# Kernel optimization log

Hardware: AMD Instinct MI355X
Metric: run time of the kernel (lower is better)

The kernel has to match this reference:

```python
import jax, jax.numpy as jnp
import numpy as np

T, B, I, H = 512, 64, 1024, 1024


def setup_inputs() -> dict:
    key = jax.random.key(0)
    ks = jax.random.split(key, 9)
    u = lambda k, shape: jax.random.uniform(k, shape, jnp.float32, -0.05, 0.05)
    return {
        "x": jax.random.normal(ks[0], (T, B, I), jnp.float32),
        "h0": jnp.zeros((B, H), jnp.float32),
        "c0": jnp.zeros((B, H), jnp.float32),
        "W_f": u(ks[1], (I + H, H)), "b_f": u(ks[2], (H,)),
        "W_i": u(ks[3], (I + H, H)), "b_i": u(ks[4], (H,)),
        "W_C": u(ks[5], (I + H, H)), "b_C": u(ks[6], (H,)),
        "W_o": u(ks[7], (I + H, H)), "b_o": u(ks[8], (H,)),
    }


def reference(x, h0, c0, W_f, b_f, W_i, b_i, W_C, b_C, W_o, b_o):
    # Fuse the 4 gate projections into one GEMM: W is [(H_prev + I), 4H]
    W = jnp.concatenate([W_f, W_i, W_C, W_o], axis=1)  # [I+H, 4H]
    b = jnp.concatenate([b_f, b_i, b_C, b_o], axis=0)  # [4H]
    Hn = h0.shape[1]

    def step(carry, x_t):
        h_t1, c_t1 = carry
        xh = jnp.concatenate([h_t1, x_t], axis=1)  # [B, H+I]
        gates = xh @ W + b                          # [B, 4H]
        f_t = jax.nn.sigmoid(gates[:, 0 * Hn:1 * Hn])
        i_t = jax.nn.sigmoid(gates[:, 1 * Hn:2 * Hn])
        g_t = jnp.tanh(gates[:, 2 * Hn:3 * Hn])
        o_t = jax.nn.sigmoid(gates[:, 3 * Hn:4 * Hn])
        c_t = f_t * c_t1 + i_t * g_t
        h_t = o_t * jnp.tanh(c_t)
        return (h_t, c_t), h_t

    (h_last, c_last), h_seq = jax.lax.scan(step, (h0, c0), x)
    return h_seq, h_last, c_last
```

## Files before the change

kernel.cpp:

```cpp
#include <hip/hip_runtime.h>

typedef unsigned short u16;
typedef unsigned int   u32;
typedef unsigned long long u64;
typedef __attribute__((ext_vector_type(8))) __bf16 bf16x8;
typedef __attribute__((ext_vector_type(4))) float  f32x4;

#define NWG    128
#define TSTEPS 512

__device__ __forceinline__ u16 f2bf(float f) {
  union { float f; u32 u; } v; v.f = f;
  return (u16)((v.u + 0x7FFFu + ((v.u >> 16) & 1u)) >> 16);
}
__device__ __forceinline__ float sigf(float x)     { return 1.f / (1.f + __expf(-x)); }
__device__ __forceinline__ float tanhfast(float x) { return 2.f / (1.f + __expf(-2.f * x)) - 1.f; }

__global__ void convert_x_kernel(const float* __restrict__ x, u16* __restrict__ xb, long n) {
  long i = (long)(blockIdx.x * blockDim.x + threadIdx.x) * 4;
  long stride = (long)gridDim.x * blockDim.x * 4;
  for (; i < n; i += stride) {
    float4 v = *reinterpret_cast<const float4*>(x + i);
    ushort4 o; o.x = f2bf(v.x); o.y = f2bf(v.y); o.z = f2bf(v.z); o.w = f2bf(v.w);
    *reinterpret_cast<ushort4*>(xb + i) = o;
  }
}

__global__ void convert_h0_tiled(const float* __restrict__ h0, u16* __restrict__ hb) {
  int gid = blockIdx.x * blockDim.x + threadIdx.x;
  int row = gid >> 9;
  int k0  = (gid & 511) << 1;
  float a = h0[row * 1024 + k0];
  float b = h0[row * 1024 + k0 + 1];
  int off = ((row >> 4) * 32 + (k0 >> 5)) * 512 + (row & 15) * 32 + ((k0 >> 3) & 3) * 8 + (k0 & 7);
  u32 hv = (u32)f2bf(a) | ((u32)f2bf(b) << 16);
  *((u32*)hb + (off >> 1)) = hv;
}

__global__ void arrange_w_kernel(const float* __restrict__ Wf, const float* __restrict__ Wi,
                                 const float* __restrict__ Wc, const float* __restrict__ Wo,
                                 u16* __restrict__ wfrag) {
  __shared__ float lds[4][512][8];
  const int n = blockIdx.x >> 2;
  const int w = blockIdx.x & 3;
  const int tid = threadIdx.x;
  #pragma unroll
  for (int g = 0; g < 4; ++g) {
    const float* W = (g == 0) ? Wf : (g == 1) ? Wi : (g == 2) ? Wc : Wo;
    for (int it = 0; it < 16; ++it) {
      int e = it * 256 + tid;
      int kk = e >> 3, jj = e & 7;
      lds[g][kk][jj] = W[(size_t)(w * 512 + kk) * 1024 + n * 8 + jj];
    }
  }
  __syncthreads();
  u16* outp = wfrag + ((size_t)blockIdx.x << 14);
  for (int it = 0; it < 64; ++it) {
    int e = it * 256 + tid;
    int b = e & 7, lane = (e >> 3) & 63, tile = (e >> 9) & 1, ks = e >> 10;
    int kk = ks * 32 + ((lane >> 4) << 3) + b;
    int c  = tile * 16 + (lane & 15);
    int g  = c >> 3, jj = c & 7;
    outp[e] = f2bf(lds[g][kk][jj]);
  }
}

__launch_bounds__(256, 1)
__global__ void lstm_main_kernel(
    const u16* __restrict__ xbf, const u16* __restrict__ wfrag,
    const float* __restrict__ c0,
    const float* __restrict__ bF, const float* __restrict__ bI,
    const float* __restrict__ bC, const float* __restrict__ bO,
    u16* __restrict__ hb, float* __restrict__ out, u32* flags)
{
  const int n    = blockIdx.x;
  const int tid  = threadIdx.x;
  const int w    = tid >> 6;
  const int lane = tid & 63;
  const int lr   = lane & 15;
  const int hi   = lane >> 4;
  const int lk   = hi << 3;

  __shared__ float part[4][64][36];

  bf16x8 bq[16][2];
  {
    const u16* wp = wfrag + ((size_t)(n * 4 + w) << 14) + lane * 8;
    #pragma unroll
    for (int ks = 0; ks < 16; ++ks) {
      bq[ks][0] = *reinterpret_cast<const bf16x8*>(wp + ks * 1024);
      bq[ks][1] = *reinterpret_cast<const bf16x8*>(wp + ks * 1024 + 512);
    }
  }

  const int erow = tid >> 2;
  const int ejj  = (tid & 3) << 1;
  const int j0   = n * 8 + ejj;
  float cR0 = c0[erow * 1024 + j0];
  float cR1 = c0[erow * 1024 + j0 + 1];
  const float bf0 = bF[j0], bf1 = bF[j0 + 1];
  const float bi0 = bI[j0], bi1 = bI[j0 + 1];
  const float bc0 = bC[j0], bc1 = bC[j0 + 1];
  const float bo0 = bO[j0], bo1 = bO[j0 + 1];
  const int hoff_u32 = (((erow >> 4) * 32 + (j0 >> 5)) * 512
                        + (erow & 15) * 32 + ((j0 >> 3) & 3) * 8 + (j0 & 7)) >> 1;

  #pragma unroll 1
  for (int t = 0; t < TSTEPS; ++t) {
    f32x4 acc[4][2];
    #pragma unroll
    for (int m = 0; m < 4; ++m) {
      acc[m][0] = (f32x4){0.f, 0.f, 0.f, 0.f};
      acc[m][1] = (f32x4){0.f, 0.f, 0.f, 0.f};
    }

    if (w < 2) {
      if (t > 0) {
        const u32 tv = (u32)t;
        while (true) {
          u32 f0 = __hip_atomic_load(flags + lane,      __ATOMIC_RELAXED, __HIP_MEMORY_SCOPE_AGENT);
          u32 f1 = __hip_atomic_load(flags + 64 + lane, __ATOMIC_RELAXED, __HIP_MEMORY_SCOPE_AGENT);
          if (__all((f0 >= tv) && (f1 >= tv))) break;
          __builtin_amdgcn_s_sleep(1);
        }
      }
      const u64* hq = (const u64*)(hb + (t & 1) * 65536);
      #pragma unroll
      for (int m = 0; m < 4; ++m) {
        union { u64 q[2]; bf16x8 v; } av[16];
        #pragma unroll
        for (int ks = 0; ks < 16; ++ks) {
          int idx = (m * 32 + w * 16 + ks) * 128 + lr * 8 + hi * 2;
          av[ks].q[0] = __hip_atomic_load(hq + idx,     __ATOMIC_RELAXED, __HIP_MEMORY_SCOPE_AGENT);
          av[ks].q[1] = __hip_atomic_load(hq + idx + 1, __ATOMIC_RELAXED, __HIP_MEMORY_SCOPE_AGENT);
        }
        #pragma unroll
        for (int ks = 0; ks < 16; ++ks) {
          acc[m][0] = __builtin_amdgcn_mfma_f32_16x16x32_bf16(av[ks].v, bq[ks][0], acc[m][0], 0, 0, 0);
          acc[m][1] = __builtin_amdgcn_mfma_f32_16x16x32_bf16(av[ks].v, bq[ks][1], acc[m][1], 0, 0, 0);
        }
      }
    } else {
      const u16* asrc = xbf + (size_t)t * 65536 + (w - 2) * 512;
      #pragma unroll
      for (int ks = 0; ks < 16; ++ks) {
        #pragma unroll
        for (int m = 0; m < 4; ++m) {
          bf16x8 av = *reinterpret_cast<const bf16x8*>(asrc + (m * 16 + lr) * 1024 + ks * 32 + lk);
          acc[m][0] = __builtin_amdgcn_mfma_f32_16x16x32_bf16(av, bq[ks][0], acc[m][0], 0, 0, 0);
          acc[m][1] = __builtin_amdgcn_mfma_f32_16x16x32_bf16(av, bq[ks][1], acc[m][1], 0, 0, 0);
        }
      }
    }

    #pragma unroll
    for (int m = 0; m < 4; ++m)
      #pragma unroll
      for (int nt = 0; nt < 2; ++nt)
        #pragma unroll
        for (int r = 0; r < 4; ++r)
          part[w][m * 16 + (hi << 2) + r][nt * 16 + lr] = acc[m][nt][r];

    __syncthreads();

    float a8[8];
    #pragma unroll
    for (int q = 0; q < 2; ++q) {
      int jj = ejj + q;
      #pragma unroll
      for (int g = 0; g < 4; ++g)
        a8[q * 4 + g] = part[0][erow][g * 8 + jj] + part[1][erow][g * 8 + jj]
                      + part[2][erow][g * 8 + jj] + part[3][erow][g * 8 + jj];
    }
    float fA = sigf(a8[0] + bf0), iA = sigf(a8[1] + bi0);
    float gA = tanhfast(a8[2] + bc0), oA = sigf(a8[3] + bo0);
    float cn0 = fA * cR0 + iA * gA;
    float hn0 = oA * tanhfast(cn0);
    cR0 = cn0;
    float fB = sigf(a8[4] + bf1), iB = sigf(a8[5] + bi1);
    float gB = tanhfast(a8[6] + bc1), oB = sigf(a8[7] + bo1);
    float cn1 = fB * cR1 + iB * gB;
    float hn1 = oB * tanhfast(cn1);
    cR1 = cn1;

    {
      u32 hv = (u32)f2bf(hn0) | ((u32)f2bf(hn1) << 16);
      u32* hdst32 = (u32*)(hb + ((t + 1) & 1) * 65536) + hoff_u32;
      __hip_atomic_store(hdst32, hv, __ATOMIC_RELAXED, __HIP_MEMORY_SCOPE_AGENT);
    }
    size_t ob = (size_t)t * 65536 + erow * 1024 + j0;
    out[ob]     = hn0;
    out[ob + 1] = hn1;
    if (t == TSTEPS - 1) {
      out[33554432 + erow * 1024 + j0]     = hn0;
      out[33554432 + erow * 1024 + j0 + 1] = hn1;
      out[33619968 + erow * 1024 + j0]     = cn0;
      out[33619968 + erow * 1024 + j0 + 1] = cn1;
    }

    __syncthreads();
    if (t < TSTEPS - 1 && tid == 0)
      __hip_atomic_store(flags + n, (u32)(t + 1), __ATOMIC_RELAXED, __HIP_MEMORY_SCOPE_AGENT);
  }
}

extern "C" void kernel_launch(void* const* d_in, const int* in_sizes, int n_in,
                              void* d_out, int out_size, void* d_ws, size_t ws_size,
                              hipStream_t stream) {
  const float* x  = (const float*)d_in[0];
  const float* h0 = (const float*)d_in[1];
  const float* c0 = (const float*)d_in[2];
  const float* Wf = (const float*)d_in[3];
  const float* bf = (const float*)d_in[4];
  const float* Wi = (const float*)d_in[5];
  const float* bi = (const float*)d_in[6];
  const float* Wc = (const float*)d_in[7];
  const float* bc = (const float*)d_in[8];
  const float* Wo = (const float*)d_in[9];
  const float* bo = (const float*)d_in[10];

  if (ws_size < ((80u << 20) + (1u << 18) + 1024)) return;
  char* ws   = (char*)d_ws;
  u16* wfrag = (u16*)ws;
  u16* xbf   = (u16*)(ws + (16u << 20));
  u16* hb    = (u16*)(ws + (80u << 20));
  u32* flags = (u32*)(ws + (80u << 20) + (1u << 18));
  float* outp = (float*)d_out;

  hipMemsetAsync(flags, 0, 512, stream);
  convert_x_kernel<<<2048, 256, 0, stream>>>(x, xbf, (long)512 * 64 * 1024);
  convert_h0_tiled<<<128, 256, 0, stream>>>(h0, hb);
  arrange_w_kernel<<<512, 256, 0, stream>>>(Wf, Wi, Wc, Wo, wfrag);

  void* args[] = {(void*)&xbf, (void*)&wfrag, (void*)&c0, (void*)&bf, (void*)&bi,
                  (void*)&bc, (void*)&bo, (void*)&hb, (void*)&outp, (void*)&flags};
  hipError_t e = hipLaunchCooperativeKernel((const void*)lstm_main_kernel, dim3(NWG),
                                            dim3(256), args, 0, stream);
  if (e != hipSuccess) {
    lstm_main_kernel<<<dim3(NWG), dim3(256), 0, stream>>>(xbf, wfrag, c0, bf, bi,
                                                          bc, bo, hb, outp, flags);
  }
}
```

Before: 5.838 ms.

## Add dedicated aggregator workgroup to publish per-step epoch for grid barrier

Adds an extra workgroup whose first wavefront polls all 128 per-workgroup flags and publishes a single epoch counter each timestep. Compute workgroups now have one wave spin on that single epoch word and relay readiness to the second wave through an LDS variable, instead of two waves each scanning 128 flags. This is meant to cut global-memory polling traffic and contention on the flag array. The cost is an extra hop of latency through the aggregator on every step and one more workgroup in the cooperative launch.

```diff
diff --git a/kernel.cpp b/kernel.cpp
--- a/kernel.cpp
+++ b/kernel.cpp
@@ -75,6 +75,24 @@
 {
   const int n    = blockIdx.x;
   const int tid  = threadIdx.x;
+  u32* const epoch = flags + 192;
+
+  if (n == NWG) {
+    if (tid < 64) {
+      for (u32 tv = 1; tv < TSTEPS; ++tv) {
+        while (true) {
+          u32 f0 = __hip_atomic_load(flags + tid,      __ATOMIC_RELAXED, __HIP_MEMORY_SCOPE_AGENT);
+          u32 f1 = __hip_atomic_load(flags + 64 + tid, __ATOMIC_RELAXED, __HIP_MEMORY_SCOPE_AGENT);
+          if (__all((f0 >= tv) && (f1 >= tv))) break;
+          __builtin_amdgcn_s_sleep(1);
+        }
+        if (tid == 0)
+          __hip_atomic_store(epoch, tv, __ATOMIC_RELAXED, __HIP_MEMORY_SCOPE_AGENT);
+      }
+    }
+    return;
+  }
+
   const int w    = tid >> 6;
   const int lane = tid & 63;
   const int lr   = lane & 15;
@@ -82,6 +100,7 @@
   const int lk   = hi << 3;
 
   __shared__ float part[4][64][36];
+  __shared__ u32 go;
 
   bf16x8 bq[16][2];
   {
@@ -92,6 +111,8 @@
       bq[ks][1] = *reinterpret_cast<const bf16x8*>(wp + ks * 1024 + 512);
     }
   }
+  if (tid == 0) go = 0;
+  __syncthreads();
 
   const int erow = tid >> 2;
   const int ejj  = (tid & 3) << 1;
@@ -117,11 +138,14 @@
     if (w < 2) {
       if (t > 0) {
         const u32 tv = (u32)t;
-        while (true) {
-          u32 f0 = __hip_atomic_load(flags + lane,      __ATOMIC_RELAXED, __HIP_MEMORY_SCOPE_AGENT);
-          u32 f1 = __hip_atomic_load(flags + 64 + lane, __ATOMIC_RELAXED, __HIP_MEMORY_SCOPE_AGENT);
-          if (__all((f0 >= tv) && (f1 >= tv))) break;
-          __builtin_amdgcn_s_sleep(1);
+        if (w == 0) {
+          while (__hip_atomic_load(epoch, __ATOMIC_RELAXED, __HIP_MEMORY_SCOPE_AGENT) < tv)
+            __builtin_amdgcn_s_sleep(4);
+          if (lane == 0)
+            __hip_atomic_store(&go, tv, __ATOMIC_RELAXED, __HIP_MEMORY_SCOPE_WORKGROUP);
+        } else {
+          while (__hip_atomic_load(&go, __ATOMIC_RELAXED, __HIP_MEMORY_SCOPE_WORKGROUP) < tv)
+            __builtin_amdgcn_s_sleep(1);
         }
       }
       const u64* hq = (const u64*)(hb + (t & 1) * 65536);
@@ -227,17 +251,17 @@
   u32* flags = (u32*)(ws + (80u << 20) + (1u << 18));
   float* outp = (float*)d_out;
 
-  hipMemsetAsync(flags, 0, 512, stream);
+  hipMemsetAsync(flags, 0, 1024, stream);
   convert_x_kernel<<<2048, 256, 0, stream>>>(x, xbf, (long)512 * 64 * 1024);
   convert_h0_tiled<<<128, 256, 0, stream>>>(h0, hb);
   arrange_w_kernel<<<512, 256, 0, stream>>>(Wf, Wi, Wc, Wo, wfrag);
 
   void* args[] = {(void*)&xbf, (void*)&wfrag, (void*)&c0, (void*)&bf, (void*)&bi,
                   (void*)&bc, (void*)&bo, (void*)&hb, (void*)&outp, (void*)&flags};
-  hipError_t e = hipLaunchCooperativeKernel((const void*)lstm_main_kernel, dim3(NWG),
+  hipError_t e = hipLaunchCooperativeKernel((const void*)lstm_main_kernel, dim3(NWG + 1),
                                             dim3(256), args, 0, stream);
   if (e != hipSuccess) {
-    lstm_main_kernel<<<dim3(NWG), dim3(256), 0, stream>>>(xbf, wfrag, c0, bf, bi,
-                                                          bc, bo, hb, outp, flags);
-  }
-}
+    lstm_main_kernel<<<dim3(NWG + 1), dim3(256), 0, stream>>>(xbf, wfrag, c0, bf, bi,
+                                                              bc, bo, hb, outp, flags);
+  }
+}
```

Result: faster. 5.316 ms (-8.9%).

## Replace per-block flag array with global arrival counter and intra-block done flags

Applied to the files above, without the earlier changes.

Replaces the per-workgroup flag array, which every waiter polled across 128 entries, with a single global counter that each workgroup atomically increments once its four waves have stored h. One wave polls the counter and signals the others through an LDS variable. The end-of-step __syncthreads is removed by double-buffering the LDS partial-sum array and using per-wave done flags. The aim is lower grid-barrier latency per timestep. The trade-off is contention on one atomic and relaxed-ordering memory visibility that is easy to get subtly wrong.

```diff
diff --git a/kernel.cpp b/kernel.cpp
--- a/kernel.cpp
+++ b/kernel.cpp
@@ -80,8 +80,11 @@
   const int lr   = lane & 15;
   const int hi   = lane >> 4;
   const int lk   = hi << 3;
-
-  __shared__ float part[4][64][36];
+  u32* const cnt = flags;
+
+  __shared__ float part[2][4][64][36];
+  __shared__ u32 done[4];
+  __shared__ u32 go;
 
   bf16x8 bq[16][2];
   {
@@ -92,6 +95,8 @@
       bq[ks][1] = *reinterpret_cast<const bf16x8*>(wp + ks * 1024 + 512);
     }
   }
+  if (tid < 4) done[tid] = 0;
+  if (tid == 0) go = 0;
 
   const int erow = tid >> 2;
   const int ejj  = (tid & 3) << 1;
@@ -104,9 +109,11 @@
   const float bo0 = bO[j0], bo1 = bO[j0 + 1];
   const int hoff_u32 = (((erow >> 4) * 32 + (j0 >> 5)) * 512
                         + (erow & 15) * 32 + ((j0 >> 3) & 3) * 8 + (j0 & 7)) >> 1;
+  __syncthreads();
 
   #pragma unroll 1
   for (int t = 0; t < TSTEPS; ++t) {
+    const int par = t & 1;
     f32x4 acc[4][2];
     #pragma unroll
     for (int m = 0; m < 4; ++m) {
@@ -116,15 +123,18 @@
 
     if (w < 2) {
       if (t > 0) {
-        const u32 tv = (u32)t;
-        while (true) {
-          u32 f0 = __hip_atomic_load(flags + lane,      __ATOMIC_RELAXED, __HIP_MEMORY_SCOPE_AGENT);
-          u32 f1 = __hip_atomic_load(flags + 64 + lane, __ATOMIC_RELAXED, __HIP_MEMORY_SCOPE_AGENT);
-          if (__all((f0 >= tv) && (f1 >= tv))) break;
-          __builtin_amdgcn_s_sleep(1);
-        }
-      }
-      const u64* hq = (const u64*)(hb + (t & 1) * 65536);
+        const u32 need = (u32)t * (u32)NWG;
+        if (w == 0) {
+          while (__hip_atomic_load(cnt, __ATOMIC_RELAXED, __HIP_MEMORY_SCOPE_AGENT) < need)
+            __builtin_amdgcn_s_sleep(2);
+          if (lane == 0)
+            __hip_atomic_store(&go, (u32)t, __ATOMIC_RELAXED, __HIP_MEMORY_SCOPE_WORKGROUP);
+        } else {
+          while (__hip_atomic_load(&go, __ATOMIC_RELAXED, __HIP_MEMORY_SCOPE_WORKGROUP) < (u32)t)
+            __builtin_amdgcn_s_sleep(1);
+        }
+      }
+      const u64* hq = (const u64*)(hb + par * 65536);
       #pragma unroll
       for (int m = 0; m < 4; ++m) {
         union { u64 q[2]; bf16x8 v; } av[16];
@@ -159,7 +169,7 @@
       for (int nt = 0; nt < 2; ++nt)
         #pragma unroll
         for (int r = 0; r < 4; ++r)
-          part[w][m * 16 + (hi << 2) + r][nt * 16 + lr] = acc[m][nt][r];
+          part[par][w][m * 16 + (hi << 2) + r][nt * 16 + lr] = acc[m][nt][r];
 
     __syncthreads();
 
@@ -169,8 +179,8 @@
       int jj = ejj + q;
       #pragma unroll
       for (int g = 0; g < 4; ++g)
-        a8[q * 4 + g] = part[0][erow][g * 8 + jj] + part[1][erow][g * 8 + jj]
-                      + part[2][erow][g * 8 + jj] + part[3][erow][g * 8 + jj];
+        a8[q * 4 + g] = part[par][0][erow][g * 8 + jj] + part[par][1][erow][g * 8 + jj]
+                      + part[par][2][erow][g * 8 + jj] + part[par][3][erow][g * 8 + jj];
     }
     float fA = sigf(a8[0] + bf0), iA = sigf(a8[1] + bi0);
     float gA = tanhfast(a8[2] + bc0), oA = sigf(a8[3] + bo0);
@@ -185,9 +195,25 @@
 
     {
       u32 hv = (u32)f2bf(hn0) | ((u32)f2bf(hn1) << 16);
-      u32* hdst32 = (u32*)(hb + ((t + 1) & 1) * 65536) + hoff_u32;
+      u32* hdst32 = (u32*)(hb + (par ^ 1) * 65536) + hoff_u32;
       __hip_atomic_store(hdst32, hv, __ATOMIC_RELAXED, __HIP_MEMORY_SCOPE_AGENT);
     }
+
+    if (t < TSTEPS - 1) {
+      asm volatile("s_waitcnt vmcnt(0)" ::: "memory");
+      __builtin_amdgcn_sched_barrier(0);
+      if (lane == 0)
+        __hip_atomic_store(&done[w], (u32)(t + 1), __ATOMIC_RELAXED, __HIP_MEMORY_SCOPE_WORKGROUP);
+      if (w == 3 && lane == 0) {
+        const u32 tv = (u32)(t + 1);
+        while (__hip_atomic_load(&done[0], __ATOMIC_RELAXED, __HIP_MEMORY_SCOPE_WORKGROUP) < tv ||
+               __hip_atomic_load(&done[1], __ATOMIC_RELAXED, __HIP_MEMORY_SCOPE_WORKGROUP) < tv ||
+               __hip_atomic_load(&done[2], __ATOMIC_RELAXED, __HIP_MEMORY_SCOPE_WORKGROUP) < tv)
+          ;
+        __hip_atomic_fetch_add(cnt, 1u, __ATOMIC_RELAXED, __HIP_MEMORY_SCOPE_AGENT);
+      }
+    }
+
     size_t ob = (size_t)t * 65536 + erow * 1024 + j0;
     out[ob]     = hn0;
     out[ob + 1] = hn1;
@@ -197,10 +223,6 @@
       out[33619968 + erow * 1024 + j0]     = cn0;
       out[33619968 + erow * 1024 + j0 + 1] = cn1;
     }
-
-    __syncthreads();
-    if (t < TSTEPS - 1 && tid == 0)
-      __hip_atomic_store(flags + n, (u32)(t + 1), __ATOMIC_RELAXED, __HIP_MEMORY_SCOPE_AGENT);
   }
 }
 
@@ -227,7 +249,7 @@
   u32* flags = (u32*)(ws + (80u << 20) + (1u << 18));
   float* outp = (float*)d_out;
 
-  hipMemsetAsync(flags, 0, 512, stream);
+  hipMemsetAsync(flags, 0, 1024, stream);
   convert_x_kernel<<<2048, 256, 0, stream>>>(x, xbf, (long)512 * 64 * 1024);
   convert_h0_tiled<<<128, 256, 0, stream>>>(h0, hb);
   arrange_w_kernel<<<512, 256, 0, stream>>>(Wf, Wi, Wc, Wo, wfrag);
```

Result: slower. 7.827 ms (+34.1%).

## Add per-XCD relay blocks that copy the hidden state into an XCD-local buffer

Applied to the files above, without the earlier changes.

Launches 64 extra relay workgroups. Up to 8 per XCD wait for all compute blocks to finish a step, copy the bf16 hidden state into a per-XCD buffer, and publish a tag. Compute blocks poll their XCD's tags and, if ready, read h from the copy through sc0 loads. This is meant to cut cross-XCD coherence traffic on the recurrent read, and they fall back to the global flag barrier after a bounded wait. The flag store is also moved ahead of the output writes, adding a relay hop of latency per step and relying on non-atomic copies being visible.

```diff
diff --git a/kernel.cpp b/kernel.cpp
--- a/kernel.cpp
+++ b/kernel.cpp
@@ -7,6 +7,7 @@
 typedef __attribute__((ext_vector_type(4))) float  f32x4;
 
 #define NWG    128
+#define NRELAY 64
 #define TSTEPS 512
 
 __device__ __forceinline__ u16 f2bf(float f) {
@@ -71,10 +72,49 @@
     const float* __restrict__ c0,
     const float* __restrict__ bF, const float* __restrict__ bI,
     const float* __restrict__ bC, const float* __restrict__ bO,
-    u16* __restrict__ hb, float* __restrict__ out, u32* flags)
+    u16* __restrict__ hb, float* __restrict__ out, u32* flags, u16* xcdbuf)
 {
   const int n    = blockIdx.x;
   const int tid  = threadIdx.x;
+  u32* const rcount = flags + 128;
+  u32* const tags   = flags + 256;
+
+  u32 xcd;
+  asm volatile("s_getreg_b32 %0, hwreg(HW_REG_XCC_ID)" : "=s"(xcd));
+  xcd &= 7;
+
+  if (n >= NWG) {
+    __shared__ u32 rr;
+    if (tid == 0)
+      rr = __hip_atomic_fetch_add(rcount + xcd, 1u, __ATOMIC_RELAXED, __HIP_MEMORY_SCOPE_AGENT);
+    __syncthreads();
+    const u32 rank = rr;
+    if (tid >= 64 || rank >= 8) return;
+    const int r = (int)rank;
+    for (int s = 1; s < TSTEPS; ++s) {
+      const u32 sv = (u32)s;
+      while (true) {
+        u32 f0 = __hip_atomic_load(flags + tid,      __ATOMIC_RELAXED, __HIP_MEMORY_SCOPE_AGENT);
+        u32 f1 = __hip_atomic_load(flags + 64 + tid, __ATOMIC_RELAXED, __HIP_MEMORY_SCOPE_AGENT);
+        if (__all((f0 >= sv) && (f1 >= sv))) break;
+        __builtin_amdgcn_s_sleep(2);
+      }
+      const u64* src = (const u64*)(hb + (s & 1) * 65536) + r * 2048;
+      u64* dst = (u64*)(xcdbuf + ((size_t)xcd * 2 + (s & 1)) * 65536) + r * 2048;
+      #pragma unroll
+      for (int i = 0; i < 16; ++i) {
+        int e = (i * 64 + tid) * 2;
+        u64 a = __hip_atomic_load(src + e,     __ATOMIC_RELAXED, __HIP_MEMORY_SCOPE_AGENT);
+        u64 b = __hip_atomic_load(src + e + 1, __ATOMIC_RELAXED, __HIP_MEMORY_SCOPE_AGENT);
+        dst[e] = a; dst[e + 1] = b;
+      }
+      asm volatile("s_waitcnt vmcnt(0)" ::: "memory");
+      if (tid == 0)
+        *(volatile u32*)(tags + xcd * 16 + r) = sv + 1;
+    }
+    return;
+  }
+
   const int w    = tid >> 6;
   const int lane = tid & 63;
   const int lr   = lane & 15;
@@ -82,7 +122,6 @@
   const int lk   = hi << 3;
 
   __shared__ float part[4][64][36];
-
   bf16x8 bq[16][2];
   {
     const u16* wp = wfrag + ((size_t)(n * 4 + w) << 14) + lane * 8;
@@ -115,29 +154,61 @@
     }
 
     if (w < 2) {
+      bool use_local = false;
       if (t > 0) {
-        const u32 tv = (u32)t;
-        while (true) {
-          u32 f0 = __hip_atomic_load(flags + lane,      __ATOMIC_RELAXED, __HIP_MEMORY_SCOPE_AGENT);
-          u32 f1 = __hip_atomic_load(flags + 64 + lane, __ATOMIC_RELAXED, __HIP_MEMORY_SCOPE_AGENT);
-          if (__all((f0 >= tv) && (f1 >= tv))) break;
+        const u32 tv1 = (u32)t + 1;
+        const u32* tagp = tags + xcd * 16 + (lane & 7);
+        for (int tries = 0; tries < 64; ++tries) {
+          u32 tg;
+          asm volatile("global_load_dword %0, %1, off sc0" : "=v"(tg) : "v"(tagp));
+          asm volatile("s_waitcnt vmcnt(0)" ::: "memory");
+          if (__all(tg >= tv1)) { use_local = true; break; }
           __builtin_amdgcn_s_sleep(1);
         }
-      }
-      const u64* hq = (const u64*)(hb + (t & 1) * 65536);
-      #pragma unroll
-      for (int m = 0; m < 4; ++m) {
-        union { u64 q[2]; bf16x8 v; } av[16];
+        if (!use_local) {
+          const u32 tv = (u32)t;
+          while (true) {
+            u32 f0 = __hip_atomic_load(flags + lane,      __ATOMIC_RELAXED, __HIP_MEMORY_SCOPE_AGENT);
+            u32 f1 = __hip_atomic_load(flags + 64 + lane, __ATOMIC_RELAXED, __HIP_MEMORY_SCOPE_AGENT);
+            if (__all((f0 >= tv) && (f1 >= tv))) break;
+            __builtin_amdgcn_s_sleep(2);
+          }
+        }
+      }
+      if (use_local) {
+        const u16* xb = xcdbuf + ((size_t)xcd * 2 + (t & 1)) * 65536;
         #pragma unroll
-        for (int ks = 0; ks < 16; ++ks) {
-          int idx = (m * 32 + w * 16 + ks) * 128 + lr * 8 + hi * 2;
-          av[ks].q[0] = __hip_atomic_load(hq + idx,     __ATOMIC_RELAXED, __HIP_MEMORY_SCOPE_AGENT);
-          av[ks].q[1] = __hip_atomic_load(hq + idx + 1, __ATOMIC_RELAXED, __HIP_MEMORY_SCOPE_AGENT);
-        }
+        for (int m = 0; m < 4; ++m) {
+          bf16x8 av[16];
+          #pragma unroll
+          for (int ks = 0; ks < 16; ++ks)
+            asm volatile("global_load_dwordx4 %0, %1, off sc0"
+                         : "=v"(av[ks])
+                         : "v"(xb + (m * 32 + w * 16 + ks) * 512 + lr * 32 + hi * 8));
+          asm volatile("s_waitcnt vmcnt(0)" ::: "memory");
+          __builtin_amdgcn_sched_barrier(0);
+          #pragma unroll
+          for (int ks = 0; ks < 16; ++ks) {
+            acc[m][0] = __builtin_amdgcn_mfma_f32_16x16x32_bf16(av[ks], bq[ks][0], acc[m][0], 0, 0, 0);
+            acc[m][1] = __builtin_amdgcn_mfma_f32_16x16x32_bf16(av[ks], bq[ks][1], acc[m][1], 0, 0, 0);
+          }
+        }
+      } else {
+        const u64* hq = (const u64*)(hb + (t & 1) * 65536);
         #pragma unroll
-        for (int ks = 0; ks < 16; ++ks) {
-          acc[m][0] = __builtin_amdgcn_mfma_f32_16x16x32_bf16(av[ks].v, bq[ks][0], acc[m][0], 0, 0, 0);
-          acc[m][1] = __builtin_amdgcn_mfma_f32_16x16x32_bf16(av[ks].v, bq[ks][1], acc[m][1], 0, 0, 0);
+        for (int m = 0; m < 4; ++m) {
+          union { u64 q[2]; bf16x8 v; } av[16];
+          #pragma unroll
+          for (int ks = 0; ks < 16; ++ks) {
+            int idx = (m * 32 + w * 16 + ks) * 128 + lr * 8 + hi * 2;
+            av[ks].q[0] = __hip_atomic_load(hq + idx,     __ATOMIC_RELAXED, __HIP_MEMORY_SCOPE_AGENT);
+            av[ks].q[1] = __hip_atomic_load(hq + idx + 1, __ATOMIC_RELAXED, __HIP_MEMORY_SCOPE_AGENT);
+          }
+          #pragma unroll
+          for (int ks = 0; ks < 16; ++ks) {
+            acc[m][0] = __builtin_amdgcn_mfma_f32_16x16x32_bf16(av[ks].v, bq[ks][0], acc[m][0], 0, 0, 0);
+            acc[m][1] = __builtin_amdgcn_mfma_f32_16x16x32_bf16(av[ks].v, bq[ks][1], acc[m][1], 0, 0, 0);
+          }
         }
       }
     } else {
@@ -188,6 +259,11 @@
       u32* hdst32 = (u32*)(hb + ((t + 1) & 1) * 65536) + hoff_u32;
       __hip_atomic_store(hdst32, hv, __ATOMIC_RELAXED, __HIP_MEMORY_SCOPE_AGENT);
     }
+
+    __syncthreads();
+    if (t < TSTEPS - 1 && tid == 0)
+      __hip_atomic_store(flags + n, (u32)(t + 1), __ATOMIC_RELAXED, __HIP_MEMORY_SCOPE_AGENT);
+
     size_t ob = (size_t)t * 65536 + erow * 1024 + j0;
     out[ob]     = hn0;
     out[ob + 1] = hn1;
@@ -197,10 +273,6 @@
       out[33619968 + erow * 1024 + j0]     = cn0;
       out[33619968 + erow * 1024 + j0 + 1] = cn1;
     }
-
-    __syncthreads();
-    if (t < TSTEPS - 1 && tid == 0)
-      __hip_atomic_store(flags + n, (u32)(t + 1), __ATOMIC_RELAXED, __HIP_MEMORY_SCOPE_AGENT);
   }
 }
 
@@ -219,25 +291,27 @@
   const float* Wo = (const float*)d_in[9];
   const float* bo = (const float*)d_in[10];
 
-  if (ws_size < ((80u << 20) + (1u << 18) + 1024)) return;
+  if (ws_size < ((80u << 20) + (1u << 18) + 2048)) return;
   char* ws   = (char*)d_ws;
   u16* wfrag = (u16*)ws;
+  u16* xcdbuf = (u16*)(ws + (14u << 20));
   u16* xbf   = (u16*)(ws + (16u << 20));
   u16* hb    = (u16*)(ws + (80u << 20));
   u32* flags = (u32*)(ws + (80u << 20) + (1u << 18));
   float* outp = (float*)d_out;
 
-  hipMemsetAsync(flags, 0, 512, stream);
+  hipMemsetAsync(flags, 0, 2048, stream);
   convert_x_kernel<<<2048, 256, 0, stream>>>(x, xbf, (long)512 * 64 * 1024);
   convert_h0_tiled<<<128, 256, 0, stream>>>(h0, hb);
   arrange_w_kernel<<<512, 256, 0, stream>>>(Wf, Wi, Wc, Wo, wfrag);
 
   void* args[] = {(void*)&xbf, (void*)&wfrag, (void*)&c0, (void*)&bf, (void*)&bi,
-                  (void*)&bc, (void*)&bo, (void*)&hb, (void*)&outp, (void*)&flags};
-  hipError_t e = hipLaunchCooperativeKernel((const void*)lstm_main_kernel, dim3(NWG),
-                                            dim3(256), args, 0, stream);
+                  (void*)&bc, (void*)&bo, (void*)&hb, (void*)&outp, (void*)&flags,
+                  (void*)&xcdbuf};
+  hipError_t e = hipLaunchCooperativeKernel((const void*)lstm_main_kernel,
+                                            dim3(NWG + NRELAY), dim3(256), args, 0, stream);
   if (e != hipSuccess) {
-    lstm_main_kernel<<<dim3(NWG), dim3(256), 0, stream>>>(xbf, wfrag, c0, bf, bi,
-                                                          bc, bo, hb, outp, flags);
-  }
-}
+    lstm_main_kernel<<<dim3(NWG + NRELAY), dim3(256), 0, stream>>>(
+        xbf, wfrag, c0, bf, bi, bc, bo, hb, outp, flags, xcdbuf);
+  }
+}
```

Result: slower. 8.748 ms (+49.9%).
